# Optimization experiments

Measured on AMD Instinct MI355X. Metric: run time of the kernel, lower is better.

## Reference

```python
import jax, jax.numpy as jnp
import numpy as np

N_NODES = 10000
N_EDGES = 320000
N_REL = 460
N_BASES = 30
D = 200


def setup_inputs() -> dict:
    key = jax.random.key(0)
    k = jax.random.split(key, 8)
    x = jax.random.normal(k[0], (N_NODES, D), dtype=jnp.float32)
    edge_index = jax.random.randint(k[1], (2, N_EDGES), 0, N_NODES, dtype=jnp.int32)
    edge_type = jax.random.randint(k[2], (N_EDGES,), 0, N_REL, dtype=jnp.int32)
    # Xavier-uniform-like init scales
    w_bound = float(np.sqrt(6.0 / (D + D)))
    c_bound = float(np.sqrt(6.0 / (N_REL + N_BASES)))
    weight = jax.random.uniform(k[3], (N_BASES, D, D), minval=-w_bound, maxval=w_bound, dtype=jnp.float32)
    coeff = jax.random.uniform(k[4], (N_REL, N_BASES), minval=-c_bound, maxval=c_bound, dtype=jnp.float32)
    self_weight = jax.random.uniform(k[5], (D, D), minval=-w_bound, maxval=w_bound, dtype=jnp.float32)
    bias = jnp.zeros((D,), dtype=jnp.float32)
    return {
        "x": x,
        "weight": weight,
        "coeff": coeff,
        "self_weight": self_weight,
        "bias": bias,
        "edge_index": edge_index,
        "edge_type": edge_type,
        "num_nodes": N_NODES,
    }


def reference(x, weight, coeff, self_weight, bias, edge_index, edge_type, num_nodes):
    # RelationalGraphConv.forward:
    #   W_r = sum_b coeff[r, b] * V_b ; msg_e = x[src_e] @ W_{type_e}
    #   out[n] = (sum_{e: tgt_e = n} msg_e) / max(in_deg[n], 1) + x @ W_self + bias
    src = edge_index[0]
    tgt = edge_index[1]
    src_feats = x[src]                    # (E, d_in) gather
    edge_coeff = coeff[edge_type]         # (E, B) gather

    # msg_e = sum_b coeff[type_e, b] * (src_e @ V_b): scan over bases to avoid
    # materializing an (E, B, d_out) intermediate (same math as W_r = coeff @ V).
    def body(acc, inputs):
        Vb, cb = inputs                   # (d_in, d_out), (E,)
        return acc + (src_feats @ Vb) * cb[:, None], None

    msg0 = jnp.zeros((src.shape[0], weight.shape[2]), dtype=x.dtype)
    msg, _ = jax.lax.scan(body, msg0, (weight, edge_coeff.T))  # (E, d_out)

    out = jax.ops.segment_sum(msg, tgt, num_segments=num_nodes)              # (N, d_out)
    deg = jax.ops.segment_sum(jnp.ones_like(tgt, dtype=x.dtype), tgt, num_segments=num_nodes)
    out = out / jnp.clip(deg, 1.0)[:, None]
    out = out + x @ self_weight + bias
    return out
```

## Files before the change

### kernel.cpp

```cpp
#include <hip/hip_runtime.h>
#include <hip/hip_bf16.h>

#define N_NODES 10000
#define N_EDGES 320000
#define N_REL   460
#define N_BASES 30
#define DIM     200
#define KZ      6016
#define KT      6240
#define NSTEPS  195
#define NTILES  157
#define NFRAG   16
#define KSPLIT  6
#define PROWS   10048
#define TKELEM  2048

#define PREP_B  (NFRAG * NSTEPS * 512)
#define PREP_C  (N_REL * 16)
#define PREP_X  (N_NODES * 224)
#define S1_TOTAL (N_EDGES + PREP_B + PREP_C)
#define S2_TOTAL (N_EDGES + PREP_X)

using short8  = __attribute__((ext_vector_type(8))) short;
using floatx4 = __attribute__((ext_vector_type(4))) float;

__device__ __forceinline__ unsigned short f2bf(float f) {
    union { float f; unsigned u; } v; v.f = f;
    unsigned u = v.u;
    return (unsigned short)((u + 0x7fffu + ((u >> 16) & 1u)) >> 16);
}

__device__ __forceinline__ short8 pack8(const unsigned short* u) {
    union { unsigned short s[8]; short8 v; } p;
#pragma unroll
    for (int i = 0; i < 8; ++i) p.s[i] = u[i];
    return p.v;
}

__device__ __forceinline__ size_t asw_idx(int n, int c) {
    int t = n >> 6, sub = (n >> 4) & 3, rl = n & 15;
    int kk = c >> 5, w = c & 31;
    return (size_t)(t * NSTEPS + kk) * TKELEM + sub * 512 + rl * 32 + w;
}


__global__ void sort1_kernel(const int* __restrict__ tgt, int* __restrict__ deg,
                             const float* __restrict__ weight, const float* __restrict__ sw,
                             const float* __restrict__ coeff,
                             unsigned short* __restrict__ BSW, unsigned int* __restrict__ Cpair) {
    int idx = blockIdx.x * blockDim.x + threadIdx.x;
    if (idx < N_EDGES) {
        atomicAdd(&deg[tgt[idx]], 1);
        return;
    }
    idx -= N_EDGES;
    if (idx < PREP_B) {
        int f = idx / (NSTEPS * 512);
        int rem = idx - f * (NSTEPS * 512);
        int kk = rem / 512;
        int e = rem - kk * 512;
        int l = e >> 3, j = e & 7;
        int rB = f * 16 + (l & 15);
        int k  = kk * 32 + (l >> 4) * 8 + j;
        float v = 0.f;
        if (rB < DIM) {
            if (k < KZ) {
                if (k < N_BASES * DIM) {
                    int b = k / DIM, kc = k - b * DIM;
                    v = weight[(b * DIM + kc) * DIM + rB];
                }
            } else {
                int jj = k - KZ;
                if (jj < DIM) v = sw[jj * DIM + rB];
            }
        }
        BSW[idx] = f2bf(v);
        return;
    }
    idx -= PREP_B;
    if (idx < PREP_C) {
        int t = idx >> 4, m = idx & 15;
        unsigned lo = f2bf(coeff[t * N_BASES + m]);
        unsigned hi = (m + 16 < N_BASES) ? f2bf(coeff[t * N_BASES + m + 16]) : 0u;
        Cpair[idx] = lo | (hi << 16);
    }
}

__global__ __launch_bounds__(1024) void scan_kernel(const int* deg, int* starts,
                                                    int* cursor, float* dinv) {
    __shared__ int part[1024];
    int tid = threadIdx.x;
    const int PER = (N_NODES + 1023) / 1024;
    int base = tid * PER;
    int s = 0;
    for (int i = 0; i < PER; ++i) { int idx = base + i; if (idx < N_NODES) s += deg[idx]; }
    part[tid] = s; __syncthreads();
    for (int off = 1; off < 1024; off <<= 1) {
        int v = (tid >= off) ? part[tid - off] : 0;
        __syncthreads();
        part[tid] += v;
        __syncthreads();
    }
    int run = (tid > 0) ? part[tid - 1] : 0;
    for (int i = 0; i < PER; ++i) {
        int idx = base + i;
        if (idx < N_NODES) {
            int d = deg[idx];
            starts[idx] = run; cursor[idx] = run;
            dinv[idx] = 1.0f / (float)(d > 0 ? d : 1);
            run += d;
        }
    }
    if (tid == 1023) starts[N_NODES] = part[1023];
}


__global__ void sort2_kernel(const int* __restrict__ src, const int* __restrict__ tgt,
                             const int* __restrict__ etype, int* __restrict__ cursor,
                             int2* __restrict__ sedge,
                             const float* __restrict__ x, const int* __restrict__ deg,
                             unsigned short* __restrict__ Xbf, unsigned short* __restrict__ ASW) {
    int idx = blockIdx.x * blockDim.x + threadIdx.x;
    if (idx < N_EDGES) {
        int t = tgt[idx];
        int pos = atomicAdd(&cursor[t], 1);
        sedge[pos] = make_int2(src[idx], etype[idx]);
        return;
    }
    idx -= N_EDGES;
    if (idx < PREP_X) {
        int n = idx / 224, j = idx - n * 224;
        float v = (j < DIM) ? x[(size_t)n * DIM + j] : 0.f;
        if (j < DIM) Xbf[(size_t)n * DIM + j] = f2bf(v);
        int d = deg[n]; if (d < 1) d = 1;
        ASW[asw_idx(n, KZ + j)] = f2bf((float)d * v);
    }
}


__global__ __launch_bounds__(256) void agg_kernel(const unsigned short* __restrict__ Xbf,
                                                  const unsigned int* __restrict__ Cpair,
                                                  const int* __restrict__ starts,
                                                  const int2* __restrict__ sedge,
                                                  unsigned short* __restrict__ ASW) {
    __shared__ __align__(16) unsigned short zbuf[4][3232];
    int lane = threadIdx.x & 63;
    int wave = threadIdx.x >> 6;
    int n = blockIdx.x * 4 + wave;
    int ln = lane & 15, q = lane >> 4;

    floatx4 acc0[13], acc1[13];
#pragma unroll
    for (int f = 0; f < 13; ++f) {
        acc0[f] = (floatx4){0.f, 0.f, 0.f, 0.f};
        acc1[f] = acc0[f];
    }

    int e0 = starts[n], e1 = starts[n + 1];
    for (int kb = e0; kb < e1; kb += 32) {
        int eb = kb + 8 * q;
        unsigned short a0v[8], a1v[8];
        int srcs[8];
#pragma unroll
        for (int j = 0; j < 8; ++j) {
            int e = eb + j;
            int ec = (e < e1) ? e : (e1 - 1);
            int2 sd = sedge[ec];
            unsigned cp = (e < e1) ? Cpair[sd.y * 16 + ln] : 0u;
            a0v[j] = (unsigned short)(cp & 0xffffu);
            a1v[j] = (unsigned short)(cp >> 16);
            srcs[j] = sd.x;
        }
        short8 A0 = pack8(a0v), A1 = pack8(a1v);

        unsigned short bv[2][8];
#pragma unroll
        for (int j = 0; j < 8; ++j)
            bv[0][j] = Xbf[(size_t)srcs[j] * DIM + ln];
#pragma unroll
        for (int f = 0; f < 13; ++f) {
            int cur = f & 1, nxt = cur ^ 1;
            if (f < 12) {
#pragma unroll
                for (int j = 0; j < 8; ++j)
                    bv[nxt][j] = Xbf[(size_t)srcs[j] * DIM + (f + 1) * 16 + ln];
            }
            short8 B = pack8(bv[cur]);
            acc0[f] = __builtin_amdgcn_mfma_f32_16x16x32_bf16(A0, B, acc0[f], 0, 0, 0);
            acc1[f] = __builtin_amdgcn_mfma_f32_16x16x32_bf16(A1, B, acc1[f], 0, 0, 0);
        }
    }

    unsigned short* zb = zbuf[wave];
    int t = n >> 6, sub = (n >> 4) & 3, rl = n & 15;
    const uint4* zb4 = (const uint4*)zb;
    uint4* dst = (uint4*)ASW;
    size_t base_u4 = (size_t)t * NSTEPS * 256 + sub * 64 + rl * 4;

#pragma unroll
    for (int f = 0; f < 13; ++f) {
        int d = f * 16 + ln;
        if (d < DIM) {
#pragma unroll
            for (int i = 0; i < 4; ++i)
                zb[(q * 4 + i) * DIM + d] = f2bf(acc0[f][i]);
        }
    }
    for (int v = lane; v < 400; v += 64) {
        int kk = v >> 2, w8 = v & 3;
        dst[base_u4 + (size_t)kk * 256 + w8] = zb4[v];
    }

    if (lane < 16) zb[2800 + lane] = 0;
#pragma unroll
    for (int f = 0; f < 13; ++f) {
        int d = f * 16 + ln;
        if (d < DIM) {
#pragma unroll
            for (int i = 0; i < 4; ++i) {
                int b1 = 16 + q * 4 + i;
                if (b1 < N_BASES) zb[(b1 - 16) * DIM + d] = f2bf(acc1[f][i]);
            }
        }
    }
    for (int v = lane; v < 352; v += 64) {
        int kk = 100 + (v >> 2), w8 = v & 3;
        dst[base_u4 + (size_t)kk * 256 + w8] = zb4[v];
    }
}


#define GITER(VLIT, BU, BL, KK)                                                        \
  {                                                                                    \
    asm volatile("s_waitcnt vmcnt(" #VLIT ")" ::: "memory");                           \
    __builtin_amdgcn_sched_barrier(0);                                                 \
    asm volatile("s_barrier" ::: "memory");                                            \
    const int kk_ = (KK);                                                              \
    const int kld_ = (kk_ + 1 < ke) ? kk_ + 1 : ke - 1;                                \
    BL[0] = *(const short8*)(pb + ((size_t)(0 * 4 * NSTEPS) + kld_) * 512);            \
    BL[1] = *(const short8*)(pb + ((size_t)(1 * 4 * NSTEPS) + kld_) * 512);            \
    BL[2] = *(const short8*)(pb + ((size_t)(2 * 4 * NSTEPS) + kld_) * 512);            \
    BL[3] = *(const short8*)(pb + ((size_t)(3 * 4 * NSTEPS) + kld_) * 512);            \
    const int kst_ = (kk_ + 7 < ke) ? kk_ + 7 : ke - 1;                                \
    __builtin_amdgcn_global_load_lds(                                                  \
        (const unsigned int*)(aswt + (size_t)kst_ * TKELEM + goff),                    \
        (unsigned int*)(ldsw + ((kk_ + 7) & 7) * 2048), 16, 0, 0);                     \
    const unsigned short* sp_ = alds + (kk_ & 7) * 2048 + pread8;                      \
    short8 av0 = *(const short8*)(sp_);                                                \
    short8 av1 = *(const short8*)(sp_ + 512);                                          \
    short8 av2 = *(const short8*)(sp_ + 1024);                                         \
    short8 av3 = *(const short8*)(sp_ + 1536);                                         \
    _Pragma("unroll")                                                                  \
    for (int i_ = 0; i_ < 4; ++i_) {                                                   \
      acc[i_][0] = __builtin_amdgcn_mfma_f32_16x16x32_bf16(av0, BU[i_], acc[i_][0], 0, 0, 0); \
      acc[i_][1] = __builtin_amdgcn_mfma_f32_16x16x32_bf16(av1, BU[i_], acc[i_][1], 0, 0, 0); \
      acc[i_][2] = __builtin_amdgcn_mfma_f32_16x16x32_bf16(av2, BU[i_], acc[i_][2], 0, 0, 0); \
      acc[i_][3] = __builtin_amdgcn_mfma_f32_16x16x32_bf16(av3, BU[i_], acc[i_][3], 0, 0, 0); \
    }                                                                                  \
  }

__global__ __launch_bounds__(256, 4) void gemm_kernel(const unsigned short* __restrict__ ASW,
                                                      const unsigned short* __restrict__ BSW,
                                                      float* __restrict__ part) {
    __shared__ __align__(16) unsigned short alds[8 * 2048];
    int tid = threadIdx.x;
    int lane = tid & 63, wave = tid >> 6;
    int tile = blockIdx.x, chunk = blockIdx.y;
    int ks = (chunk * NSTEPS) / KSPLIT;
    int ke = ((chunk + 1) * NSTEPS) / KSPLIT;
    int ln = lane & 15, q = lane >> 4;

    const unsigned short* aswt = ASW + (size_t)tile * NSTEPS * TKELEM;
    const unsigned short* pb = BSW + (size_t)(wave * NSTEPS) * 512 + lane * 8;

    int gsw = (tid & 0xE0) | ((tid & 7) << 2) | ((tid >> 3) & 3);
    int goff = gsw * 8;
    int pread8 = ((((ln >> 3) & 1) << 5) | (q << 3) | (ln & 7)) * 8;
    unsigned short* ldsw = alds + wave * 512;

    floatx4 acc[4][4];
#pragma unroll
    for (int i = 0; i < 4; ++i)
#pragma unroll
        for (int s = 0; s < 4; ++s) acc[i][s] = (floatx4){0.f, 0.f, 0.f, 0.f};

    short8 bA[4], bB[4];

#pragma unroll
    for (int i = 0; i < 4; ++i)
        bA[i] = *(const short8*)(pb + ((size_t)(i * 4 * NSTEPS) + ks) * 512);
#pragma unroll
    for (int d = 0; d < 7; ++d)
        __builtin_amdgcn_global_load_lds(
            (const unsigned int*)(aswt + (size_t)(ks + d) * TKELEM + goff),
            (unsigned int*)(ldsw + ((ks + d) & 7) * 2048), 16, 0, 0);

    GITER(0,  bA, bB, ks + 0);
    GITER(5,  bB, bA, ks + 1);
    GITER(10, bA, bB, ks + 2);
    GITER(15, bB, bA, ks + 3);
    GITER(20, bA, bB, ks + 4);
    GITER(25, bB, bA, ks + 5);

    int kk = ks + 6;
    for (; kk + 1 < ke; kk += 2) {
        GITER(30, bA, bB, kk);
        GITER(30, bB, bA, kk + 1);
    }
    if (kk < ke) { GITER(30, bA, bB, kk); }

    int row0 = tile * 64;
    float* pbase = part + ((size_t)chunk * PROWS + row0) * 208;
#pragma unroll
    for (int i = 0; i < 4; ++i) {
        int fg = wave + 4 * i;
        if (fg < 13) {
            int c = fg * 16 + ln;
#pragma unroll
            for (int s = 0; s < 4; ++s)
#pragma unroll
                for (int ii = 0; ii < 4; ++ii)
                    pbase[(s * 16 + q * 4 + ii) * 208 + c] = acc[i][s][ii];
        }
    }
}


__global__ __launch_bounds__(256) void reduce_kernel(const float* __restrict__ part,
                                                     const float* __restrict__ dinv,
                                                     const float* __restrict__ bias,
                                                     float* __restrict__ out) {
    int idx = blockIdx.x * blockDim.x + threadIdx.x;
    if (idx >= N_NODES * 50) return;
    int r = idx / 50, cq = idx - r * 50;
    float4 s = {0.f, 0.f, 0.f, 0.f};
#pragma unroll
    for (int c = 0; c < KSPLIT; ++c) {
        float4 v = *(const float4*)(part + ((size_t)c * PROWS + r) * 208 + cq * 4);
        s.x += v.x; s.y += v.y; s.z += v.z; s.w += v.w;
    }
    float dv = dinv[r];
    float4 b = *(const float4*)(bias + cq * 4);
    float4 o;
    o.x = s.x * dv + b.x; o.y = s.y * dv + b.y;
    o.z = s.z * dv + b.z; o.w = s.w * dv + b.w;
    *(float4*)(out + (size_t)r * DIM + cq * 4) = o;
}


extern "C" void kernel_launch(void* const* d_in, const int* in_sizes, int n_in,
                              void* d_out, int out_size, void* d_ws, size_t ws_size,
                              hipStream_t stream) {
    const float* x      = (const float*)d_in[0];
    const float* weight = (const float*)d_in[1];
    const float* coeff  = (const float*)d_in[2];
    const float* selfw  = (const float*)d_in[3];
    const float* bias   = (const float*)d_in[4];
    const int*   eidx   = (const int*)d_in[5];
    const int*   etype  = (const int*)d_in[6];
    const int* src = eidx;
    const int* tgt = eidx + N_EDGES;
    float* out = (float*)d_out;

    char* ws = (char*)d_ws;
    size_t off = 0;
    auto carve = [&](size_t bytes) {
        char* p = ws + off;
        off += (bytes + 255) & ~(size_t)255;
        return p;
    };
    unsigned short* ASW  = (unsigned short*)carve((size_t)NTILES * NSTEPS * TKELEM * 2);
    unsigned short* BSW  = (unsigned short*)carve((size_t)NFRAG * NSTEPS * 512 * 2);
    float* part   = (float*)carve((size_t)KSPLIT * PROWS * 208 * 4);
    unsigned short* Xbf  = (unsigned short*)carve((size_t)(N_NODES * DIM + 64) * 2);
    unsigned int*  Cpair = (unsigned int*)carve((size_t)N_REL * 16 * 4);
    int*   deg    = (int*)carve((size_t)N_NODES * 4);
    int*   starts = (int*)carve((size_t)(N_NODES + 1) * 4);
    int*   cursor = (int*)carve((size_t)N_NODES * 4);
    float* dinv   = (float*)carve((size_t)N_NODES * 4);
    int2*  sedge  = (int2*)carve((size_t)N_EDGES * 8);

    hipMemsetAsync(deg, 0, (size_t)N_NODES * 4, stream);

    sort1_kernel<<<(S1_TOTAL + 255) / 256, 256, 0, stream>>>(
        tgt, deg, weight, selfw, coeff, BSW, Cpair);

    scan_kernel<<<1, 1024, 0, stream>>>(deg, starts, cursor, dinv);

    sort2_kernel<<<(S2_TOTAL + 255) / 256, 256, 0, stream>>>(
        src, tgt, etype, cursor, sedge, x, deg, Xbf, ASW);

    agg_kernel<<<N_NODES / 4, 256, 0, stream>>>(Xbf, Cpair, starts, sedge, ASW);

    dim3 ggrid(NTILES, KSPLIT);
    gemm_kernel<<<ggrid, 256, 0, stream>>>(ASW, BSW, part);

    reduce_kernel<<<(N_NODES * 50 + 255) / 256, 256, 0, stream>>>(part, dinv, bias, out);
}
```

Measured before the change: 253.1 us.

## Triple-buffer B fragments in registers and issue loads after MFMAs

Changes the B-operand register prefetch in the GEMM main loop from double buffering one step ahead to triple buffering three steps ahead. The global B loads and the LDS A prefetch are now issued after the MFMA block instead of before it. The waitcnt thresholds are retuned to match the new load ordering. This is meant to hide global B-load latency behind more compute, at the cost of extra VGPRs, which may pressure occupancy under launch_bounds(256,4).

```diff
diff --git a/kernel.cpp b/kernel.cpp
--- a/kernel.cpp
+++ b/kernel.cpp
@@ -230,21 +230,12 @@
 }
 
 
-#define GITER(VLIT, BU, BL, KK)                                                        \
+#define GITER(VLIT, BX, KK)                                                            \
   {                                                                                    \
     asm volatile("s_waitcnt vmcnt(" #VLIT ")" ::: "memory");                           \
     __builtin_amdgcn_sched_barrier(0);                                                 \
     asm volatile("s_barrier" ::: "memory");                                            \
     const int kk_ = (KK);                                                              \
-    const int kld_ = (kk_ + 1 < ke) ? kk_ + 1 : ke - 1;                                \
-    BL[0] = *(const short8*)(pb + ((size_t)(0 * 4 * NSTEPS) + kld_) * 512);            \
-    BL[1] = *(const short8*)(pb + ((size_t)(1 * 4 * NSTEPS) + kld_) * 512);            \
-    BL[2] = *(const short8*)(pb + ((size_t)(2 * 4 * NSTEPS) + kld_) * 512);            \
-    BL[3] = *(const short8*)(pb + ((size_t)(3 * 4 * NSTEPS) + kld_) * 512);            \
-    const int kst_ = (kk_ + 7 < ke) ? kk_ + 7 : ke - 1;                                \
-    __builtin_amdgcn_global_load_lds(                                                  \
-        (const unsigned int*)(aswt + (size_t)kst_ * TKELEM + goff),                    \
-        (unsigned int*)(ldsw + ((kk_ + 7) & 7) * 2048), 16, 0, 0);                     \
     const unsigned short* sp_ = alds + (kk_ & 7) * 2048 + pread8;                      \
     short8 av0 = *(const short8*)(sp_);                                                \
     short8 av1 = *(const short8*)(sp_ + 512);                                          \
@@ -252,11 +243,20 @@
     short8 av3 = *(const short8*)(sp_ + 1536);                                         \
     _Pragma("unroll")                                                                  \
     for (int i_ = 0; i_ < 4; ++i_) {                                                   \
-      acc[i_][0] = __builtin_amdgcn_mfma_f32_16x16x32_bf16(av0, BU[i_], acc[i_][0], 0, 0, 0); \
-      acc[i_][1] = __builtin_amdgcn_mfma_f32_16x16x32_bf16(av1, BU[i_], acc[i_][1], 0, 0, 0); \
-      acc[i_][2] = __builtin_amdgcn_mfma_f32_16x16x32_bf16(av2, BU[i_], acc[i_][2], 0, 0, 0); \
-      acc[i_][3] = __builtin_amdgcn_mfma_f32_16x16x32_bf16(av3, BU[i_], acc[i_][3], 0, 0, 0); \
+      acc[i_][0] = __builtin_amdgcn_mfma_f32_16x16x32_bf16(av0, BX[i_], acc[i_][0], 0, 0, 0); \
+      acc[i_][1] = __builtin_amdgcn_mfma_f32_16x16x32_bf16(av1, BX[i_], acc[i_][1], 0, 0, 0); \
+      acc[i_][2] = __builtin_amdgcn_mfma_f32_16x16x32_bf16(av2, BX[i_], acc[i_][2], 0, 0, 0); \
+      acc[i_][3] = __builtin_amdgcn_mfma_f32_16x16x32_bf16(av3, BX[i_], acc[i_][3], 0, 0, 0); \
     }                                                                                  \
+    const int kld_ = (kk_ + 3 < ke) ? kk_ + 3 : ke - 1;                                \
+    BX[0] = *(const short8*)(pb + ((size_t)(0 * 4 * NSTEPS) + kld_) * 512);            \
+    BX[1] = *(const short8*)(pb + ((size_t)(1 * 4 * NSTEPS) + kld_) * 512);            \
+    BX[2] = *(const short8*)(pb + ((size_t)(2 * 4 * NSTEPS) + kld_) * 512);            \
+    BX[3] = *(const short8*)(pb + ((size_t)(3 * 4 * NSTEPS) + kld_) * 512);            \
+    const int kst_ = (kk_ + 7 < ke) ? kk_ + 7 : ke - 1;                                \
+    __builtin_amdgcn_global_load_lds(                                                  \
+        (const unsigned int*)(aswt + (size_t)kst_ * TKELEM + goff),                    \
+        (unsigned int*)(ldsw + ((kk_ + 7) & 7) * 2048), 16, 0, 0);                     \
   }
 
 __global__ __launch_bounds__(256, 4) void gemm_kernel(const unsigned short* __restrict__ ASW,
@@ -284,30 +284,37 @@
 #pragma unroll
         for (int s = 0; s < 4; ++s) acc[i][s] = (floatx4){0.f, 0.f, 0.f, 0.f};
 
-    short8 bA[4], bB[4];
-
-#pragma unroll
-    for (int i = 0; i < 4; ++i)
-        bA[i] = *(const short8*)(pb + ((size_t)(i * 4 * NSTEPS) + ks) * 512);
+    short8 b0[4], b1[4], b2[4];
+
+#pragma unroll
+    for (int i = 0; i < 4; ++i) {
+        b0[i] = *(const short8*)(pb + ((size_t)(i * 4 * NSTEPS) + ks) * 512);
+        b1[i] = *(const short8*)(pb + ((size_t)(i * 4 * NSTEPS) + ks + 1) * 512);
+        b2[i] = *(const short8*)(pb + ((size_t)(i * 4 * NSTEPS) + ks + 2) * 512);
+    }
+    __builtin_amdgcn_sched_barrier(0);
 #pragma unroll
     for (int d = 0; d < 7; ++d)
         __builtin_amdgcn_global_load_lds(
             (const unsigned int*)(aswt + (size_t)(ks + d) * TKELEM + goff),
             (unsigned int*)(ldsw + ((ks + d) & 7) * 2048), 16, 0, 0);
-
-    GITER(0,  bA, bB, ks + 0);
-    GITER(5,  bB, bA, ks + 1);
-    GITER(10, bA, bB, ks + 2);
-    GITER(15, bB, bA, ks + 3);
-    GITER(20, bA, bB, ks + 4);
-    GITER(25, bB, bA, ks + 5);
+    __builtin_amdgcn_sched_barrier(0);
+
+    GITER(6,  b0, ks + 0);
+    GITER(10, b1, ks + 1);
+    GITER(14, b2, ks + 2);
+    GITER(18, b0, ks + 3);
+    GITER(22, b1, ks + 4);
+    GITER(26, b2, ks + 5);
 
     int kk = ks + 6;
-    for (; kk + 1 < ke; kk += 2) {
-        GITER(30, bA, bB, kk);
-        GITER(30, bB, bA, kk + 1);
-    }
-    if (kk < ke) { GITER(30, bA, bB, kk); }
+    for (; kk + 2 < ke; kk += 3) {
+        GITER(30, b0, kk);
+        GITER(30, b1, kk + 1);
+        GITER(30, b2, kk + 2);
+    }
+    if (kk < ke)     { GITER(30, b0, kk); }
+    if (kk + 1 < ke) { GITER(30, b1, kk + 1); }
 
     int row0 = tile * 64;
     float* pbase = part + ((size_t)chunk * PROWS + row0) * 208;
```

Measured after the change: 461.4 us. 1.82x slower.
